# Kernel optimization log

Hardware: AMD Instinct MI355X
Metric: run time of the kernel (lower is better)

## Reference

```python
import jax, jax.numpy as jnp
import numpy as np

H = 64        # hidden_size
G = 64        # global_hidden_size
VOCAB = 128   # VOCAB_SIZE
NUM_OPS = 20
DEPTH = 12    # complete binary tree: 2**DEPTH - 1 nodes
B = 128       # batch of trees
TEMP = 3.0    # self.temperature


def setup_inputs() -> dict:
    key = jax.random.key(0)
    ks = jax.random.split(key, 16)
    s = 0.05
    N = 2 ** DEPTH - 1
    inp = {
        "x_idx": jax.random.randint(ks[0], (B, N), 0, VOCAB, dtype=jnp.int32),
        "validity_mask": jnp.ones((NUM_OPS,), jnp.float32),
        # binary tree-LSTM (blstm): x one-hot -> gates [i, f_a, f_b, o, u]
        "Wx": jax.random.normal(ks[1], (VOCAB, 5 * H), jnp.float32) * s,
        "Ua": jax.random.normal(ks[2], (H, 5 * H), jnp.float32) * s,
        "Ub": jax.random.normal(ks[3], (H, 5 * H), jnp.float32) * s,
        "b_tree": jnp.zeros((5 * H,), jnp.float32),
        # global nn.LSTM (1 layer), gate order i,f,g,o
        "W_ih": jax.random.normal(ks[4], (H, 4 * G), jnp.float32) * s,
        "W_hh": jax.random.normal(ks[5], (G, 4 * G), jnp.float32) * s,
        "b_lstm": jnp.zeros((4 * G,), jnp.float32),
        # FFN on root hidden
        "W1": jax.random.normal(ks[6], (H, H), jnp.float32) * s,
        "b1": jnp.zeros((H,), jnp.float32),
        "W2": jax.random.normal(ks[7], (H, H), jnp.float32) * s,
        "b2": jnp.zeros((H,), jnp.float32),
        # actor head on [hidden ; global_hidden]
        "actor_W": jax.random.normal(ks[8], (H + G, NUM_OPS), jnp.float32) * s,
        "actor_b": jnp.zeros((NUM_OPS,), jnp.float32),
    }
    return inp


def _tree_lstm_sweep(x_idx, Wx, Ua, Ub, b_tree):
    """Bottom-up binary tree-LSTM over a complete binary tree.
    Node i's children sit at flat positions 2i+1, 2i+2 (level layout)."""
    h_prev = c_prev = None
    for d in range(DEPTH - 1, -1, -1):
        n = 2 ** d
        off = n - 1
        # memory-bound gather of gate pre-activations: [B, n, 5H]
        z = Wx[x_idx[:, off:off + n]] + b_tree
        if h_prev is not None:
            h_a, h_b = h_prev[:, 0::2], h_prev[:, 1::2]
            c_a, c_b = c_prev[:, 0::2], c_prev[:, 1::2]
            z = z + jnp.einsum("bnh,hg->bng", h_a, Ua) + jnp.einsum("bnh,hg->bng", h_b, Ub)
        i, fa, fb, o, u = jnp.split(z, 5, axis=-1)
        c = jax.nn.sigmoid(i) * jnp.tanh(u)
        if h_prev is not None:
            c = c + jax.nn.sigmoid(fa) * c_a + jax.nn.sigmoid(fb) * c_b
        h = jax.nn.sigmoid(o) * jnp.tanh(c)
        h_prev, c_prev = h, c
    return h_prev[:, 0]  # root hidden [B, H]


def reference(x_idx, validity_mask, Wx, Ua, Ub, b_tree, W_ih, W_hh, b_lstm,
              W1, b1, W2, b2, actor_W, actor_b):
    h_root = _tree_lstm_sweep(x_idx, Wx, Ua, Ub, b_tree)
    # internal op 1: apply_ffn then apply_global_lstm
    f = jnp.maximum(h_root @ W1 + b1, 0.0) @ W2 + b2          # FFN [B, H]
    h0 = jnp.zeros((f.shape[0], G), f.dtype)
    g = f @ W_ih + h0 @ W_hh + b_lstm                          # one LSTM step
    i, fg, gg, o = jnp.split(g, 4, axis=-1)                    # torch order i,f,g,o
    c_g = jax.nn.sigmoid(i) * jnp.tanh(gg)                     # c0 = 0
    h_g = jax.nn.sigmoid(o) * jnp.tanh(c_g)                    # [B, G]
    # external actor with validity-masked weights (as in policy())
    feats = jnp.concatenate([f, h_g], axis=-1)                 # [B, H+G]
    logits = jnp.log(validity_mask) + feats @ (actor_W * validity_mask) + actor_b * validity_mask
    return jax.nn.softmax(logits / TEMP, axis=-1)              # [B, NUM_OPS]
```

## Files before the change

### kernel.cpp

```cpp
#include <hip/hip_runtime.h>


typedef unsigned short u16;
typedef unsigned int   u32;
typedef __attribute__((ext_vector_type(8))) short  short8;
typedef __attribute__((ext_vector_type(4))) float  floatx4;

#define L2E  1.44269504f
#define L2E2 2.885390082f

__device__ __forceinline__ float frcp(float x) { return __fdividef(1.0f, x); }
__device__ __forceinline__ float fsig(float x) { return frcp(1.0f + __expf(-x)); }
__device__ __forceinline__ float ftanh(float x) {
    return 1.0f - 2.0f * frcp(__expf(2.0f * x) + 1.0f);
}
__device__ __forceinline__ u16 f2bfa(float x) {
    return (u16)((__float_as_uint(x) + 0x8000u) >> 16);
}
__device__ __forceinline__ float bflo(u32 cc) { return __uint_as_float(cc << 16); }
__device__ __forceinline__ float bfhi(u32 cc) { return __uint_as_float(cc & 0xFFFF0000u); }
__device__ __forceinline__ float bf2f(u16 s) { return __uint_as_float(((u32)s) << 16); }

__device__ __forceinline__ void lstm_gates(
    float zi, float zfa, float zfb, float zo, float zu,
    float ca, float cb, float& c, float& h)
{
    zi  = fmaxf(zi, -60.f);  zfa = fmaxf(zfa, -60.f);
    zfb = fmaxf(zfb, -60.f); zo  = fmaxf(zo, -60.f);
    zu  = fmaxf(zu, -60.f);
    float ei  = __builtin_amdgcn_exp2f(-zi);
    float efa = __builtin_amdgcn_exp2f(-zfa);
    float efb = __builtin_amdgcn_exp2f(-zfb);
    float eo  = __builtin_amdgcn_exp2f(-zo);
    float eu2 = __builtin_amdgcn_exp2f(-zu);
    float pfa = 1.f + efa, pfb = 1.f + efb;
    float cf = (ca * pfb + cb * pfa) * __builtin_amdgcn_rcpf(pfa * pfb);
    c = (1.f - eu2) * __builtin_amdgcn_rcpf((1.f + ei) * (1.f + eu2)) + cf;
    float ec2 = __builtin_amdgcn_exp2f(fminf(-c * L2E2, 80.f));
    h = (1.f - ec2) * __builtin_amdgcn_rcpf((1.f + eo) * (1.f + ec2));
}

#define HS 72

__global__ void precompute_kernel(
    const float* __restrict__ Wx, const float* __restrict__ b_tree,
    const float* __restrict__ Ua, const float* __restrict__ Ub,
    float4* __restrict__ WpA, float* __restrict__ WpU,
    float4* __restrict__ TaA, float2* __restrict__ TaUC,
    float4* __restrict__ TbA, float2* __restrict__ TbUC,
    u16* __restrict__ Uswz, float* __restrict__ Us)
{
    int v = blockIdx.x;
    int t = threadIdx.x;
    __shared__ float sz[320], sta[320], stb[320], sh[64], sc[64];
    float z = Wx[v * 320 + t] + b_tree[t];
    sz[t] = z;
    {
        int f = v * 320 + t;
        int j = f & 7, lane = (f >> 3) & 63, tk = f >> 9;
        int nt = tk % 20, kc = tk / 20;
        int k = kc * 32 + (lane >> 4) * 8 + j;
        int nn = nt * 16 + (lane & 15);
        float uval = (k < 64) ? Ua[k * 320 + nn] : Ub[(k - 64) * 320 + nn];
        uval *= ((nn >> 6) == 4) ? L2E2 : L2E;
        Uswz[f] = (u16)((__float_as_uint(uval) + 0x7FFFu +
                         ((__float_as_uint(uval) >> 16) & 1u)) >> 16);
    }
    {
        float uval = (v < 64) ? Ua[v * 320 + t] : Ub[(v - 64) * 320 + t];
        Us[v * 320 + t] = uval * ((t >= 256) ? L2E2 : L2E);
    }
    __syncthreads();
    if (t < 64) {
        float c = fsig(sz[t]) * ftanh(sz[256 + t]);
        float h = fsig(sz[192 + t]) * ftanh(c);
        sc[t] = c; sh[t] = h;
    }
    __syncthreads();
    float ta = 0.f, tb = 0.f;
    #pragma unroll 8
    for (int k = 0; k < 64; ++k) {
        ta += sh[k] * Ua[k * 320 + t];
        tb += sh[k] * Ub[k * 320 + t];
    }
    sta[t] = ta; stb[t] = tb;
    __syncthreads();
    if (t < 64) {
        int o = (v << 6) + t;
        WpA[o]  = make_float4(sz[t] * L2E, sz[64 + t] * L2E,
                              sz[128 + t] * L2E, sz[192 + t] * L2E);
        WpU[o]  = sz[256 + t] * L2E2;
        TaA[o]  = make_float4(sta[t] * L2E, sta[64 + t] * L2E,
                              sta[128 + t] * L2E, sta[192 + t] * L2E);
        TaUC[o] = make_float2(sta[256 + t] * L2E2, sc[t]);
        TbA[o]  = make_float4(stb[t] * L2E, stb[64 + t] * L2E,
                              stb[128 + t] * L2E, stb[192 + t] * L2E);
        TbUC[o] = make_float2(stb[256 + t] * L2E2, sc[t]);
    }
}

template<int NT, int MODE, int GSRC>
__device__ __forceinline__ void sweep_level(
    const u16* hsrc, const u32* csrc,
    u16* hdst, u16* cdst, u16* hg, u16* cg, float* hroot,
    const short8 Bfrag[4][5],
    const float4* __restrict__ WpA, const float* __restrict__ WpU,
    const u16* ids, int lbase, int node0g, int nvalid,
    int lane15, int quad, int wg)
{
    floatx4 acc[NT][5];
    #pragma unroll
    for (int mt = 0; mt < NT; ++mt)
        #pragma unroll
        for (int g = 0; g < 5; ++g) acc[mt][g] = (floatx4){0.f, 0.f, 0.f, 0.f};

    #pragma unroll
    for (int mt = 0; mt < NT; ++mt) {
        #pragma unroll
        for (int kc = 0; kc < 4; ++kc) {
            int child = 2 * (lbase + mt * 16 + lane15) + (kc >> 1);
            const u16* ap = GSRC ? (hsrc + child * 64 + (kc & 1) * 32 + quad * 8)
                                 : (hsrc + child * HS + (kc & 1) * 32 + quad * 8);
            short8 a = *(const short8*)ap;
            #pragma unroll
            for (int g = 0; g < 5; ++g)
                acc[mt][g] = __builtin_amdgcn_mfma_f32_16x16x32_bf16(
                    a, Bfrag[kc][g], acc[mt][g], 0, 0, 0);
        }
    }
    int hh = wg * 16 + lane15;
    #pragma unroll
    for (int mt = 0; mt < NT; ++mt) {
        #pragma unroll
        for (int r = 0; r < 4; ++r) {
            int lrow = lbase + mt * 16 + quad * 4 + r;
            int id = ids[lrow];
            float4 wgv = WpA[(id << 6) + hh];
            float  wu  = WpU[(id << 6) + hh];
            u32 cc = csrc[lrow * 64 + hh];
            float c, h;
            lstm_gates(acc[mt][0][r] + wgv.x, acc[mt][1][r] + wgv.y,
                       acc[mt][2][r] + wgv.z, acc[mt][3][r] + wgv.w,
                       acc[mt][4][r] + wu, bflo(cc), bfhi(cc), c, h);
            if (MODE == 0) {
                hdst[lrow * HS + hh] = f2bfa(h);
                cdst[(lrow >> 1) * 128 + hh * 2 + (lrow & 1)] = f2bfa(c);
            }
            if (MODE == 1) {
                if (lrow < nvalid) {
                    int node = node0g + lrow;
                    hg[node * 64 + hh] = f2bfa(h);
                    cg[(node >> 1) * 128 + hh * 2 + (node & 1)] = f2bfa(c);
                }
            }
            if (MODE == 2) {
                if (lrow == 0) hroot[hh] = h;
            }
        }
    }
}

__device__ __forceinline__ void load_bfrags(short8 Bfrag[4][5],
                                            const u16* __restrict__ Uswz,
                                            int wg, int lane)
{
    #pragma unroll
    for (int kc = 0; kc < 4; ++kc)
        #pragma unroll
        for (int g = 0; g < 5; ++g) {
            int nt = g * 4 + wg;
            Bfrag[kc][g] = *(const short8*)(Uswz + ((kc * 20 + nt) * 64 + lane) * 8);
        }
}

__global__ __launch_bounds__(512, 2) void sweepA_kernel(
    const int* __restrict__ x_idx,
    const float4* __restrict__ WpA, const float* __restrict__ WpU,
    const float4* __restrict__ TaA, const float2* __restrict__ TaUC,
    const float4* __restrict__ TbA, const float2* __restrict__ TbUC,
    const u16* __restrict__ Uswz,
    u16* __restrict__ h3, u16* __restrict__ c3)
{
    __shared__ u16 hA[128 * HS];
    __shared__ u16 cA[64 * 128];
    __shared__ u16 hB[64 * HS];
    __shared__ u16 cB[32 * 128];
    __shared__ u16 sIds[544];
    int t = threadIdx.x, lane = t & 63, wv = t >> 6;
    int wg = wv & 3, wm = wv >> 2;
    int lane15 = lane & 15, quad = lane >> 4;
    int b = blockIdx.x >> 3, st = blockIdx.x & 7;
    const int* xb = x_idx + b * 4095;

    for (int i = t; i < 544; i += 512) {
        int g;
        if      (i < 128) g = 1023 + st * 128 + i;
        else if (i < 384) g = 2047 + st * 256 + (i - 128);
        else if (i < 448) g = 511 + st * 64 + (i - 384);
        else if (i < 480) g = 255 + st * 32 + (i - 448);
        else if (i < 496) g = 127 + st * 16 + (i - 480);
        else if (i < 504) g = 63 + st * 8 + (i - 496);
        else if (i < 508) g = 31 + st * 4 + (i - 504);
        else if (i < 510) g = 15 + st * 2 + (i - 508);
        else if (i == 510) g = 7 + st;
        else g = -1;
        sIds[i] = (g >= 0) ? (u16)xb[g] : (u16)0;
    }
    __syncthreads();

    #pragma unroll 4
    for (int rr = 0; rr < 16; ++rr) {
        int rl = wv * 16 + rr;
        int id = sIds[rl], ida = sIds[128 + 2 * rl], idb = sIds[129 + 2 * rl];
        float4 wgv = WpA[(id << 6) + lane];  float  wu = WpU[(id << 6) + lane];
        float4 ga = TaA[(ida << 6) + lane];  float2 ua = TaUC[(ida << 6) + lane];
        float4 gb = TbA[(idb << 6) + lane];  float2 ub = TbUC[(idb << 6) + lane];
        float c, h;
        lstm_gates(wgv.x + ga.x + gb.x, wgv.y + ga.y + gb.y, wgv.z + ga.z + gb.z,
                   wgv.w + ga.w + gb.w, wu + ua.x + ub.x, ua.y, ub.y, c, h);
        hA[rl * HS + lane] = f2bfa(h);
        cA[(rl >> 1) * 128 + lane * 2 + (rl & 1)] = f2bfa(c);
    }
    short8 Bfrag[4][5];
    load_bfrags(Bfrag, Uswz, wg, lane);
    __syncthreads();
    sweep_level<2, 0, 0>(hA, (const u32*)cA, hB, cB, nullptr, nullptr, nullptr,
                         Bfrag, WpA, WpU, &sIds[384], wm * 32, 0, 64, lane15, quad, wg);
    __syncthreads();
    sweep_level<1, 0, 0>(hB, (const u32*)cB, hA, cA, nullptr, nullptr, nullptr,
                         Bfrag, WpA, WpU, &sIds[448], wm * 16, 0, 32, lane15, quad, wg);
    __syncthreads();
    if (wm == 0)
        sweep_level<1, 0, 0>(hA, (const u32*)cA, hB, cB, nullptr, nullptr, nullptr,
                             Bfrag, WpA, WpU, &sIds[480], 0, 0, 16, lane15, quad, wg);
    __syncthreads();
    if (wm == 0)
        sweep_level<1, 0, 0>(hB, (const u32*)cB, hA, cA, nullptr, nullptr, nullptr,
                             Bfrag, WpA, WpU, &sIds[496], 0, 0, 8, lane15, quad, wg);
    __syncthreads();
    if (wm == 0)
        sweep_level<1, 0, 0>(hA, (const u32*)cA, hB, cB, nullptr, nullptr, nullptr,
                             Bfrag, WpA, WpU, &sIds[504], 0, 0, 4, lane15, quad, wg);
    __syncthreads();
    if (wm == 0)
        sweep_level<1, 0, 0>(hB, (const u32*)cB, hA, cA, nullptr, nullptr, nullptr,
                             Bfrag, WpA, WpU, &sIds[508], 0, 0, 2, lane15, quad, wg);
    __syncthreads();
    if (wm == 0)
        sweep_level<1, 1, 0>(hA, (const u32*)cA, nullptr, nullptr,
                             h3 + (size_t)b * 512, c3 + (size_t)b * 512, nullptr,
                             Bfrag, WpA, WpU, &sIds[510], 0, st, 1, lane15, quad, wg);
}

template<int NR>
__device__ __forceinline__ void dot_level(
    const float* __restrict__ Us, const float4* __restrict__ WpA,
    const float* __restrict__ WpU, const int* __restrict__ xb,
    const float* srch, const float* srcc,
    float* dsth, float* dstc, float* hrootv, int lane)
{
    int off = NR - 1;
    float z[NR][5];
    #pragma unroll
    for (int r = 0; r < NR; ++r) {
        int id = xb[off + r];
        float4 wgv = WpA[(id << 6) + lane];
        z[r][0] = wgv.x; z[r][1] = wgv.y; z[r][2] = wgv.z; z[r][3] = wgv.w;
        z[r][4] = WpU[(id << 6) + lane];
    }
    #pragma unroll 4
    for (int k = 0; k < 128; ++k) {
        const float* uk = Us + k * 320 + lane;
        float u0 = uk[0], u1 = uk[64], u2 = uk[128], u3 = uk[192], u4 = uk[256];
        #pragma unroll
        for (int r = 0; r < NR; ++r) {
            float hk = srch[(2 * r + (k >> 6)) * 64 + (k & 63)];
            z[r][0] += u0 * hk; z[r][1] += u1 * hk; z[r][2] += u2 * hk;
            z[r][3] += u3 * hk; z[r][4] += u4 * hk;
        }
    }
    #pragma unroll
    for (int r = 0; r < NR; ++r) {
        float c, h;
        lstm_gates(z[r][0], z[r][1], z[r][2], z[r][3], z[r][4],
                   srcc[(2 * r) * 64 + lane], srcc[(2 * r + 1) * 64 + lane], c, h);
        if (NR == 1) *hrootv = h;
        else { dsth[r * 64 + lane] = h; dstc[r * 64 + lane] = c; }
    }
}

__global__ __launch_bounds__(64) void sweepB_kernel(
    const int* __restrict__ x_idx,
    const float4* __restrict__ WpA, const float* __restrict__ WpU,
    const float* __restrict__ Us,
    const u16* __restrict__ h3, const u16* __restrict__ c3,
    const float* __restrict__ W1, const float* __restrict__ b1,
    const float* __restrict__ W2, const float* __restrict__ b2,
    const float* __restrict__ W_ih, const float* __restrict__ b_lstm,
    const float* __restrict__ actor_W, const float* __restrict__ actor_b,
    const float* __restrict__ vm, float* __restrict__ out)
{
    __shared__ float shA[8 * 64], scA[8 * 64];
    __shared__ float shB[4 * 64], scB[4 * 64];
    int lane = threadIdx.x;
    int b = blockIdx.x;
    const int* xb = x_idx + b * 4095;
    const u16* h3b = h3 + (size_t)b * 512;
    const u16* c3b = c3 + (size_t)b * 512;

    #pragma unroll
    for (int n = 0; n < 8; ++n) {
        shA[n * 64 + lane] = bf2f(h3b[n * 64 + lane]);
        scA[n * 64 + lane] = bf2f(c3b[(n >> 1) * 128 + lane * 2 + (n & 1)]);
    }
    __syncthreads();

    float hrootv = 0.f;
    dot_level<4>(Us, WpA, WpU, xb, shA, scA, shB, scB, nullptr, lane);
    __syncthreads();
    dot_level<2>(Us, WpA, WpU, xb, shB, scB, shA, scA, nullptr, lane);
    __syncthreads();
    dot_level<1>(Us, WpA, WpU, xb, shA, scA, nullptr, nullptr, &hrootv, lane);

    {
        float a = b1[lane];
        #pragma unroll 8
        for (int k = 0; k < 64; ++k) a += __shfl(hrootv, k) * W1[k * 64 + lane];
        float r1 = fmaxf(a, 0.f);
        float f = b2[lane];
        #pragma unroll 8
        for (int k = 0; k < 64; ++k) f += __shfl(r1, k) * W2[k * 64 + lane];
        float gi = b_lstm[lane], gg = b_lstm[128 + lane], go = b_lstm[192 + lane];
        #pragma unroll 8
        for (int k = 0; k < 64; ++k) {
            float fk = __shfl(f, k);
            gi += fk * W_ih[k * 256 + lane];
            gg += fk * W_ih[k * 256 + 128 + lane];
            go += fk * W_ih[k * 256 + 192 + lane];
        }
        float cg = fsig(gi) * ftanh(gg);
        float hg = fsig(go) * ftanh(cg);
        int tt = (lane < 20) ? lane : 19;
        float dot = 0.f;
        #pragma unroll 8
        for (int k = 0; k < 64; ++k) {
            float fk = __shfl(f, k), hk = __shfl(hg, k);
            dot += fk * actor_W[k * 20 + tt] + hk * actor_W[(64 + k) * 20 + tt];
        }
        float m = vm[tt];
        float lg = logf(m) + dot * m + actor_b[tt] * m;
        float mx = -1e30f;
        #pragma unroll
        for (int j = 0; j < 20; ++j) mx = fmaxf(mx, __shfl(lg, j));
        float s = 0.f;
        #pragma unroll
        for (int j = 0; j < 20; ++j) s += __expf((__shfl(lg, j) - mx) * (1.0f / 3.0f));
        if (lane < 20) out[b * 20 + lane] = __expf((lg - mx) * (1.0f / 3.0f)) / s;
    }
}

extern "C" void kernel_launch(void* const* d_in, const int* in_sizes, int n_in,
                              void* d_out, int out_size, void* d_ws, size_t ws_size,
                              hipStream_t stream)
{
    const int*   x_idx   = (const int*)d_in[0];
    const float* vm      = (const float*)d_in[1];
    const float* Wx      = (const float*)d_in[2];
    const float* Ua      = (const float*)d_in[3];
    const float* Ub      = (const float*)d_in[4];
    const float* b_tree  = (const float*)d_in[5];
    const float* W_ih    = (const float*)d_in[6];
    const float* b_lstm  = (const float*)d_in[8];
    const float* W1      = (const float*)d_in[9];
    const float* b1      = (const float*)d_in[10];
    const float* W2      = (const float*)d_in[11];
    const float* b2      = (const float*)d_in[12];
    const float* actor_W = (const float*)d_in[13];
    const float* actor_b = (const float*)d_in[14];
    float* out = (float*)d_out;

    char* ws = (char*)d_ws;
    float4* WpA  = (float4*)ws;  ws += 128 * 64 * 16;
    float4* TaA  = (float4*)ws;  ws += 128 * 64 * 16;
    float4* TbA  = (float4*)ws;  ws += 128 * 64 * 16;
    float2* TaUC = (float2*)ws;  ws += 128 * 64 * 8;
    float2* TbUC = (float2*)ws;  ws += 128 * 64 * 8;
    float*  WpU  = (float*)ws;   ws += 128 * 64 * 4;
    float*  Us   = (float*)ws;   ws += 128 * 320 * 4;
    u16*    h3   = (u16*)ws;     ws += 128 * 512 * 2;
    u16*    c3   = (u16*)ws;     ws += 128 * 512 * 2;
    u16*    Uswz = (u16*)ws;     ws += 128 * 320 * 2;

    precompute_kernel<<<128, 320, 0, stream>>>(Wx, b_tree, Ua, Ub,
                                               WpA, WpU, TaA, TaUC, TbA, TbUC,
                                               Uswz, Us);
    sweepA_kernel<<<1024, 512, 0, stream>>>(x_idx, WpA, WpU, TaA, TaUC,
                                            TbA, TbUC, Uswz, h3, c3);
    sweepB_kernel<<<128, 64, 0, stream>>>(x_idx, WpA, WpU, Us, h3, c3,
                                          W1, b1, W2, b2, W_ih, b_lstm,
                                          actor_W, actor_b, vm, out);
}
```

Baseline: 182.4 us.

## Compute first internal level via MFMA on gathered leaf states instead of vocab tables

Drops the per-vocab precomputed child projections (TaA/TbA/TaUC/TbUC) and the scalar 64-step dot products in the precompute kernel. The precompute kernel now stores each vocab entry's leaf hidden state (bf16) and cell state. The first internal level in sweepA becomes an MFMA level whose A operands are gathered by leaf token id. This shortens precompute and cuts table gather traffic, at the cost of extra MFMA work and bf16 rounding of leaf hidden states in that level.

```diff
diff --git a/kernel.cpp b/kernel.cpp
--- a/kernel.cpp
+++ b/kernel.cpp
@@ -46,13 +46,12 @@
     const float* __restrict__ Wx, const float* __restrict__ b_tree,
     const float* __restrict__ Ua, const float* __restrict__ Ub,
     float4* __restrict__ WpA, float* __restrict__ WpU,
-    float4* __restrict__ TaA, float2* __restrict__ TaUC,
-    float4* __restrict__ TbA, float2* __restrict__ TbUC,
-    u16* __restrict__ Uswz, float* __restrict__ Us)
+    u16* __restrict__ Uswz, float* __restrict__ Us,
+    u16* __restrict__ leafH, float* __restrict__ leafC)
 {
     int v = blockIdx.x;
     int t = threadIdx.x;
-    __shared__ float sz[320], sta[320], stb[320], sh[64], sc[64];
+    __shared__ float sz[320];
     float z = Wx[v * 320 + t] + b_tree[t];
     sz[t] = z;
     {
@@ -74,34 +73,19 @@
     if (t < 64) {
         float c = fsig(sz[t]) * ftanh(sz[256 + t]);
         float h = fsig(sz[192 + t]) * ftanh(c);
-        sc[t] = c; sh[t] = h;
-    }
-    __syncthreads();
-    float ta = 0.f, tb = 0.f;
-    #pragma unroll 8
-    for (int k = 0; k < 64; ++k) {
-        ta += sh[k] * Ua[k * 320 + t];
-        tb += sh[k] * Ub[k * 320 + t];
-    }
-    sta[t] = ta; stb[t] = tb;
-    __syncthreads();
-    if (t < 64) {
+        leafC[(v << 6) + t] = c;
+        leafH[(v << 6) + t] = f2bfa(h);
         int o = (v << 6) + t;
-        WpA[o]  = make_float4(sz[t] * L2E, sz[64 + t] * L2E,
-                              sz[128 + t] * L2E, sz[192 + t] * L2E);
-        WpU[o]  = sz[256 + t] * L2E2;
-        TaA[o]  = make_float4(sta[t] * L2E, sta[64 + t] * L2E,
-                              sta[128 + t] * L2E, sta[192 + t] * L2E);
-        TaUC[o] = make_float2(sta[256 + t] * L2E2, sc[t]);
-        TbA[o]  = make_float4(stb[t] * L2E, stb[64 + t] * L2E,
-                              stb[128 + t] * L2E, stb[192 + t] * L2E);
-        TbUC[o] = make_float2(stb[256 + t] * L2E2, sc[t]);
-    }
-}
-
-template<int NT, int MODE, int GSRC>
+        WpA[o] = make_float4(sz[t] * L2E, sz[64 + t] * L2E,
+                             sz[128 + t] * L2E, sz[192 + t] * L2E);
+        WpU[o] = sz[256 + t] * L2E2;
+    }
+}
+
+template<int NT, int MODE, int ASRC, int CSRC>
 __device__ __forceinline__ void sweep_level(
     const u16* hsrc, const u32* csrc,
+    const u16* lids, const float* __restrict__ leafC,
     u16* hdst, u16* cdst, u16* hg, u16* cg, float* hroot,
     const short8 Bfrag[4][5],
     const float4* __restrict__ WpA, const float* __restrict__ WpU,
@@ -119,8 +103,15 @@
         #pragma unroll
         for (int kc = 0; kc < 4; ++kc) {
             int child = 2 * (lbase + mt * 16 + lane15) + (kc >> 1);
-            const u16* ap = GSRC ? (hsrc + child * 64 + (kc & 1) * 32 + quad * 8)
-                                 : (hsrc + child * HS + (kc & 1) * 32 + quad * 8);
+            const u16* ap;
+            if (ASRC == 2) {
+                int id = lids[child];
+                ap = hsrc + id * 64 + (kc & 1) * 32 + quad * 8;
+            } else if (ASRC == 1) {
+                ap = hsrc + child * 64 + (kc & 1) * 32 + quad * 8;
+            } else {
+                ap = hsrc + child * HS + (kc & 1) * 32 + quad * 8;
+            }
             short8 a = *(const short8*)ap;
             #pragma unroll
             for (int g = 0; g < 5; ++g)
@@ -137,11 +128,18 @@
             int id = ids[lrow];
             float4 wgv = WpA[(id << 6) + hh];
             float  wu  = WpU[(id << 6) + hh];
-            u32 cc = csrc[lrow * 64 + hh];
+            float ca, cb;
+            if (CSRC == 1) {
+                ca = leafC[((int)lids[2 * lrow] << 6) + hh];
+                cb = leafC[((int)lids[2 * lrow + 1] << 6) + hh];
+            } else {
+                u32 cc = csrc[lrow * 64 + hh];
+                ca = bflo(cc); cb = bfhi(cc);
+            }
             float c, h;
             lstm_gates(acc[mt][0][r] + wgv.x, acc[mt][1][r] + wgv.y,
                        acc[mt][2][r] + wgv.z, acc[mt][3][r] + wgv.w,
-                       acc[mt][4][r] + wu, bflo(cc), bfhi(cc), c, h);
+                       acc[mt][4][r] + wu, ca, cb, c, h);
             if (MODE == 0) {
                 hdst[lrow * HS + hh] = f2bfa(h);
                 cdst[(lrow >> 1) * 128 + hh * 2 + (lrow & 1)] = f2bfa(c);
@@ -176,8 +174,7 @@
 __global__ __launch_bounds__(512, 2) void sweepA_kernel(
     const int* __restrict__ x_idx,
     const float4* __restrict__ WpA, const float* __restrict__ WpU,
-    const float4* __restrict__ TaA, const float2* __restrict__ TaUC,
-    const float4* __restrict__ TbA, const float2* __restrict__ TbUC,
+    const u16* __restrict__ leafH, const float* __restrict__ leafC,
     const u16* __restrict__ Uswz,
     u16* __restrict__ h3, u16* __restrict__ c3)
 {
@@ -206,50 +203,51 @@
         else g = -1;
         sIds[i] = (g >= 0) ? (u16)xb[g] : (u16)0;
     }
-    __syncthreads();
-
-    #pragma unroll 4
-    for (int rr = 0; rr < 16; ++rr) {
-        int rl = wv * 16 + rr;
-        int id = sIds[rl], ida = sIds[128 + 2 * rl], idb = sIds[129 + 2 * rl];
-        float4 wgv = WpA[(id << 6) + lane];  float  wu = WpU[(id << 6) + lane];
-        float4 ga = TaA[(ida << 6) + lane];  float2 ua = TaUC[(ida << 6) + lane];
-        float4 gb = TbA[(idb << 6) + lane];  float2 ub = TbUC[(idb << 6) + lane];
-        float c, h;
-        lstm_gates(wgv.x + ga.x + gb.x, wgv.y + ga.y + gb.y, wgv.z + ga.z + gb.z,
-                   wgv.w + ga.w + gb.w, wu + ua.x + ub.x, ua.y, ub.y, c, h);
-        hA[rl * HS + lane] = f2bfa(h);
-        cA[(rl >> 1) * 128 + lane * 2 + (rl & 1)] = f2bfa(c);
-    }
     short8 Bfrag[4][5];
     load_bfrags(Bfrag, Uswz, wg, lane);
     __syncthreads();
-    sweep_level<2, 0, 0>(hA, (const u32*)cA, hB, cB, nullptr, nullptr, nullptr,
-                         Bfrag, WpA, WpU, &sIds[384], wm * 32, 0, 64, lane15, quad, wg);
-    __syncthreads();
-    sweep_level<1, 0, 0>(hB, (const u32*)cB, hA, cA, nullptr, nullptr, nullptr,
-                         Bfrag, WpA, WpU, &sIds[448], wm * 16, 0, 32, lane15, quad, wg);
-    __syncthreads();
-    if (wm == 0)
-        sweep_level<1, 0, 0>(hA, (const u32*)cA, hB, cB, nullptr, nullptr, nullptr,
-                             Bfrag, WpA, WpU, &sIds[480], 0, 0, 16, lane15, quad, wg);
-    __syncthreads();
-    if (wm == 0)
-        sweep_level<1, 0, 0>(hB, (const u32*)cB, hA, cA, nullptr, nullptr, nullptr,
-                             Bfrag, WpA, WpU, &sIds[496], 0, 0, 8, lane15, quad, wg);
-    __syncthreads();
-    if (wm == 0)
-        sweep_level<1, 0, 0>(hA, (const u32*)cA, hB, cB, nullptr, nullptr, nullptr,
-                             Bfrag, WpA, WpU, &sIds[504], 0, 0, 4, lane15, quad, wg);
-    __syncthreads();
-    if (wm == 0)
-        sweep_level<1, 0, 0>(hB, (const u32*)cB, hA, cA, nullptr, nullptr, nullptr,
-                             Bfrag, WpA, WpU, &sIds[508], 0, 0, 2, lane15, quad, wg);
-    __syncthreads();
-    if (wm == 0)
-        sweep_level<1, 1, 0>(hA, (const u32*)cA, nullptr, nullptr,
-                             h3 + (size_t)b * 512, c3 + (size_t)b * 512, nullptr,
-                             Bfrag, WpA, WpU, &sIds[510], 0, st, 1, lane15, quad, wg);
+
+    sweep_level<2, 0, 2, 1>(leafH, nullptr, &sIds[128], leafC, hA, cA,
+                            nullptr, nullptr, nullptr, Bfrag, WpA, WpU,
+                            &sIds[0], wm * 64, 0, 128, lane15, quad, wg);
+    sweep_level<2, 0, 2, 1>(leafH, nullptr, &sIds[128], leafC, hA, cA,
+                            nullptr, nullptr, nullptr, Bfrag, WpA, WpU,
+                            &sIds[0], wm * 64 + 32, 0, 128, lane15, quad, wg);
+    __syncthreads();
+    sweep_level<2, 0, 0, 0>(hA, (const u32*)cA, nullptr, nullptr, hB, cB,
+                            nullptr, nullptr, nullptr, Bfrag, WpA, WpU,
+                            &sIds[384], wm * 32, 0, 64, lane15, quad, wg);
+    __syncthreads();
+    sweep_level<1, 0, 0, 0>(hB, (const u32*)cB, nullptr, nullptr, hA, cA,
+                            nullptr, nullptr, nullptr, Bfrag, WpA, WpU,
+                            &sIds[448], wm * 16, 0, 32, lane15, quad, wg);
+    __syncthreads();
+    if (wm == 0)
+        sweep_level<1, 0, 0, 0>(hA, (const u32*)cA, nullptr, nullptr, hB, cB,
+                                nullptr, nullptr, nullptr, Bfrag, WpA, WpU,
+                                &sIds[480], 0, 0, 16, lane15, quad, wg);
+    __syncthreads();
+    if (wm == 0)
+        sweep_level<1, 0, 0, 0>(hB, (const u32*)cB, nullptr, nullptr, hA, cA,
+                                nullptr, nullptr, nullptr, Bfrag, WpA, WpU,
+                                &sIds[496], 0, 0, 8, lane15, quad, wg);
+    __syncthreads();
+    if (wm == 0)
+        sweep_level<1, 0, 0, 0>(hA, (const u32*)cA, nullptr, nullptr, hB, cB,
+                                nullptr, nullptr, nullptr, Bfrag, WpA, WpU,
+                                &sIds[504], 0, 0, 4, lane15, quad, wg);
+    __syncthreads();
+    if (wm == 0)
+        sweep_level<1, 0, 0, 0>(hB, (const u32*)cB, nullptr, nullptr, hA, cA,
+                                nullptr, nullptr, nullptr, Bfrag, WpA, WpU,
+                                &sIds[508], 0, 0, 2, lane15, quad, wg);
+    __syncthreads();
+    if (wm == 0)
+        sweep_level<1, 1, 0, 0>(hA, (const u32*)cA, nullptr, nullptr,
+                                nullptr, nullptr,
+                                h3 + (size_t)b * 512, c3 + (size_t)b * 512,
+                                nullptr, Bfrag, WpA, WpU,
+                                &sIds[510], 0, st, 1, lane15, quad, wg);
 }
 
 template<int NR>
@@ -380,22 +378,19 @@
     float* out = (float*)d_out;
 
     char* ws = (char*)d_ws;
-    float4* WpA  = (float4*)ws;  ws += 128 * 64 * 16;
-    float4* TaA  = (float4*)ws;  ws += 128 * 64 * 16;
-    float4* TbA  = (float4*)ws;  ws += 128 * 64 * 16;
-    float2* TaUC = (float2*)ws;  ws += 128 * 64 * 8;
-    float2* TbUC = (float2*)ws;  ws += 128 * 64 * 8;
-    float*  WpU  = (float*)ws;   ws += 128 * 64 * 4;
-    float*  Us   = (float*)ws;   ws += 128 * 320 * 4;
-    u16*    h3   = (u16*)ws;     ws += 128 * 512 * 2;
-    u16*    c3   = (u16*)ws;     ws += 128 * 512 * 2;
-    u16*    Uswz = (u16*)ws;     ws += 128 * 320 * 2;
+    float4* WpA   = (float4*)ws;  ws += 128 * 64 * 16;
+    float*  WpU   = (float*)ws;   ws += 128 * 64 * 4;
+    float*  Us    = (float*)ws;   ws += 128 * 320 * 4;
+    float*  leafC = (float*)ws;   ws += 128 * 64 * 4;
+    u16*    leafH = (u16*)ws;     ws += 128 * 64 * 2;
+    u16*    h3    = (u16*)ws;     ws += 128 * 512 * 2;
+    u16*    c3    = (u16*)ws;     ws += 128 * 512 * 2;
+    u16*    Uswz  = (u16*)ws;     ws += 128 * 320 * 2;
 
     precompute_kernel<<<128, 320, 0, stream>>>(Wx, b_tree, Ua, Ub,
-                                               WpA, WpU, TaA, TaUC, TbA, TbUC,
-                                               Uswz, Us);
-    sweepA_kernel<<<1024, 512, 0, stream>>>(x_idx, WpA, WpU, TaA, TaUC,
-                                            TbA, TbUC, Uswz, h3, c3);
+                                               WpA, WpU, Uswz, Us, leafH, leafC);
+    sweepA_kernel<<<1024, 512, 0, stream>>>(x_idx, WpA, WpU, leafH, leafC,
+                                            Uswz, h3, c3);
     sweepB_kernel<<<128, 64, 0, stream>>>(x_idx, WpA, WpU, Us, h3, c3,
                                           W1, b1, W2, b2, W_ih, b_lstm,
                                           actor_W, actor_b, vm, out);
```

New measurement: 189.4 us. 1.04x slower.
